# Optimization experiments

Hardware: AMD Instinct MI355X
Metric: run time of the kernel (lower is better)

The kernel has to match this reference:

```python
import jax, jax.numpy as jnp
import numpy as np

NVOC, NIN, NHID = 10000, 1024, 256
T, B = 128, 64


def setup_inputs() -> dict:
    key = jax.random.key(0)
    ks = jax.random.split(key, 12)

    def nrm(k, shape, s=0.05):
        return (jax.random.normal(k, shape) * s).astype(jnp.float32)

    z = lambda *s: jnp.zeros(s, jnp.float32)
    att_scale = 2.0 / np.sqrt(NHID)
    return {
        "tokens": jax.random.randint(ks[0], (T, B), 0, NVOC),
        "E": nrm(ks[1], (NVOC, NIN), 0.1),            # embedding table
        "Wih1": nrm(ks[2], (3 * NHID, NIN)),          # GRU1 input weights (r,z,n)
        "Whh1": nrm(ks[3], (3 * NHID, NHID)),
        "bih1": z(3 * NHID), "bhh1": z(3 * NHID),
        "Wih2": nrm(ks[4], (3 * NHID, NHID + NIN)),   # GRU2 input weights
        "Whh2": nrm(ks[5], (3 * NHID, NHID)),
        "bih2": z(3 * NHID), "bhh2": z(3 * NHID),
        "Wh": nrm(ks[6], (NHID, NHID)), "bh": z(NHID),   # attention linear_hid
        "Wi": nrm(ks[7], (NHID, NHID)), "bi": z(NHID),   # attention linear_input
        "w_att": nrm(ks[8], (NHID,), att_scale),          # attention score vector
        "Wd": nrm(ks[9], (NVOC, NHID), 0.1), "bd": z(NVOC),  # decoder
    }


def _gru_cell(h, xg, Whh, bhh):
    # xg: [B, 3H] precomputed input gates; PyTorch gate order (r, z, n)
    H = h.shape[-1]
    hg = h @ Whh.T + bhh
    r = jax.nn.sigmoid(xg[:, :H] + hg[:, :H])
    zt = jax.nn.sigmoid(xg[:, H:2 * H] + hg[:, H:2 * H])
    n = jnp.tanh(xg[:, 2 * H:] + r * hg[:, 2 * H:])
    return (1.0 - zt) * n + zt * h


def reference(tokens, E, Wih1, Whh1, bih1, bhh1, Wih2, Whh2, bih2, bhh2,
              Wh, bh, Wi, bi, w_att, Wd, bd):
    Tn, Bn = tokens.shape
    H = Whh1.shape[-1]
    emb = E[tokens]                                  # [T,B,NIN] (dropout = eval identity)

    # ---- rnn_1 over full sequence ----
    xg1 = emb @ Wih1.T + bih1                        # [T,B,3H]
    def step1(h, xg_t):
        h_new = _gru_cell(h, xg_t, Whh1, bhh1)
        return h_new, h_new
    h1, out1 = jax.lax.scan(step1, jnp.zeros((Bn, H), emb.dtype), xg1)
    # h1: final hidden [B,H]; out1: [T,B,H]

    # linear_hid on rnn_1 outputs (prefix slices of this equal per-step recompute)
    proj = out1 @ Wh.T + bh                          # [T,B,H]
    tidx = jnp.arange(Tn)
    neg_inf = jnp.asarray(-jnp.inf, proj.dtype)

    # ---- decode loop with growing-window additive attention ----
    def step2(h2, inputs):
        t, emb_t = inputs
        q = h2 @ Wi.T + bi                           # [B,H]
        scores = jnp.sum(jnp.tanh(proj + q[None]) * w_att, axis=2)   # [T,B]
        scores = jnp.where(tidx[:, None] <= t, scores, neg_inf)
        energy = jax.nn.softmax(scores, axis=0)      # [T,B], prefix softmax
        # hidden[:i+1] with nlayers=1 is always the [1,B,H] final rnn_1 hidden
        state = jnp.sum(energy[:, :, None] * h1[None], axis=0)       # [B,H]
        x = jnp.concatenate([state, emb_t], axis=1)  # [B, H+NIN]
        xg = x @ Wih2.T + bih2
        h2_new = _gru_cell(h2, xg, Whh2, bhh2)
        return h2_new, h2_new                        # pred == new hidden (1-layer GRU)

    _, preds = jax.lax.scan(step2, jnp.zeros((Bn, H), emb.dtype), (tidx, emb))
    # decoder (dropout = identity in eval)
    logits = preds @ Wd.T + bd                       # [T,B,NVOC]
    return logits, h1[None]                          # hidden returned as [1,B,H]
```

## Files before the change

### kernel.cpp

```cpp
#include <hip/hip_runtime.h>
#include <cstdint>
#include <cstddef>

#define DI __device__ __forceinline__

typedef short bf16x8 __attribute__((ext_vector_type(8)));
typedef float f32x4  __attribute__((ext_vector_type(4)));
typedef _Float16 half2v __attribute__((ext_vector_type(2)));

typedef const uint32_t __attribute__((address_space(1)))* gptr_t;
typedef uint32_t       __attribute__((address_space(3)))* lptr_t;

DI void load_lds16(const void* g, void* l_wave_uniform) {
#if __has_builtin(__builtin_amdgcn_global_load_lds)
  __builtin_amdgcn_global_load_lds((gptr_t)g, (lptr_t)l_wave_uniform, 16, 0, 0);
#else
  int lane = threadIdx.x & 63;
  *(uint4*)((char*)l_wave_uniform + lane * 16) = *(const uint4*)g;
#endif
}

DI ushort f2bf(float f) {
  uint32_t u = __builtin_bit_cast(uint32_t, f);
  u += 0x7fffu + ((u >> 16) & 1u);
  return (ushort)(u >> 16);
}

DI half2v h2cast(uint32_t u) { return __builtin_bit_cast(half2v, u); }

#if __has_builtin(__builtin_amdgcn_fdot2)
#define FDOT2(a, b, c) __builtin_amdgcn_fdot2((a), (b), (c), false)
#else
DI float fdot2_fb(half2v a, half2v b, float c) {
  return c + (float)a.x * (float)b.x + (float)a.y * (float)b.y;
}
#define FDOT2(a, b, c) fdot2_fb((a), (b), (c))
#endif


__global__ void cvt_w1cat(const float* __restrict__ W1, const float* __restrict__ W2,
                          ushort* __restrict__ dst) {
  int idx = blockIdx.x * 256 + threadIdx.x;
  int e = idx * 4;
  int row = e >> 10;
  int col = e & 1023;
  const float* src = (row < 768) ? (W1 + (size_t)row * 1024 + col)
                                 : (W2 + (size_t)(row - 768) * 1280 + 256 + col);
  float4 f = *(const float4*)src;
  ushort4 o; o.x = f2bf(f.x); o.y = f2bf(f.y); o.z = f2bf(f.z); o.w = f2bf(f.w);
  *(ushort4*)(dst + e) = o;
}

__global__ void cvt_wd(const float* __restrict__ Wd, ushort* __restrict__ dst) {
  int idx = blockIdx.x * 256 + threadIdx.x;
  int e = idx * 4;
  int row = e >> 8;
  int col = e & 255;
  ushort4 o;
  if (row < 10000) {
    float4 f = *(const float4*)(Wd + (size_t)row * 256 + col);
    o.x = f2bf(f.x); o.y = f2bf(f.y); o.z = f2bf(f.z); o.w = f2bf(f.w);
  } else {
    o.x = 0; o.y = 0; o.z = 0; o.w = 0;
  }
  *(ushort4*)(dst + e) = o;
}

__global__ void cvt_whh(const float* __restrict__ W, uint32_t* __restrict__ dst) {
  int idx = blockIdx.x * 256 + threadIdx.x;
  int row = idx >> 7;
  int p = idx & 127;
  float2 f = *(const float2*)(W + (size_t)row * 256 + p * 2);
  half2v h; h.x = (_Float16)f.x; h.y = (_Float16)f.y;
  dst[idx] = __builtin_bit_cast(uint32_t, h);
}

__global__ void gather_emb(const int* __restrict__ tok, const float* __restrict__ E,
                           ushort* __restrict__ emb) {
  int row = blockIdx.x;
  int t = threadIdx.x;
  int v = tok[row];
  float4 f = *((const float4*)(E + (size_t)v * 1024) + t);
  ushort4 o; o.x = f2bf(f.x); o.y = f2bf(f.y); o.z = f2bf(f.z); o.w = f2bf(f.w);
  *((ushort4*)(emb + (size_t)row * 1024) + t) = o;
}

template <bool BIAS, bool GUARD>
__global__ __launch_bounds__(256) void gemm_bt(
    const ushort* __restrict__ A, const ushort* __restrict__ B,
    float* __restrict__ C, const float* __restrict__ bias, int M, int K, int Nout) {
  __shared__ __align__(16) ushort As[128 * 64];
  __shared__ __align__(16) ushort Bs[128 * 64];
  const int t = threadIdx.x;
  const int wave = t >> 6, lane = t & 63;
  const int m0 = blockIdx.x * 128, n0 = blockIdx.y * 128;
  const int RM = (wave >> 1) * 64, RN = (wave & 1) * 64;
  const int lm = lane & 15, kg = lane >> 4;

  f32x4 acc[4][4] = {};

  for (int k0 = 0; k0 < K; k0 += 64) {
#pragma unroll
    for (int i = 0; i < 4; ++i) {
      int off = i * 4096 + t * 16;
      int row = off >> 7;
      int colb = off & 127;
      int ub = i * 4096 + wave * 1024;
      const ushort* ga = A + (size_t)(m0 + row) * K + k0 + (colb >> 1);
      load_lds16(ga, (char*)As + ub);
      const ushort* gb = B + (size_t)(n0 + row) * K + k0 + (colb >> 1);
      load_lds16(gb, (char*)Bs + ub);
    }
    __syncthreads();
#pragma unroll
    for (int kk = 0; kk < 64; kk += 32) {
      bf16x8 af[4], bfr[4];
#pragma unroll
      for (int i = 0; i < 4; ++i) {
        af[i]  = *(const bf16x8*)(As + (RM + i * 16 + lm) * 64 + kk + kg * 8);
        bfr[i] = *(const bf16x8*)(Bs + (RN + i * 16 + lm) * 64 + kk + kg * 8);
      }
#pragma unroll
      for (int i = 0; i < 4; ++i)
#pragma unroll
        for (int j = 0; j < 4; ++j)
          acc[i][j] = __builtin_amdgcn_mfma_f32_16x16x32_bf16(af[i], bfr[j], acc[i][j], 0, 0, 0);
    }
    __syncthreads();
  }

  const int rg = lane >> 4;
#pragma unroll
  for (int i = 0; i < 4; ++i) {
    int grow = m0 + RM + i * 16 + rg * 4;
#pragma unroll
    for (int j = 0; j < 4; ++j) {
      int gcol = n0 + RN + j * 16 + lm;
      if (GUARD && gcol >= Nout) continue;
      float bv = BIAS ? bias[gcol] : 0.f;
#pragma unroll
      for (int r = 0; r < 4; ++r)
        C[(size_t)(grow + r) * Nout + gcol] = acc[i][j][r] + bv;
    }
  }
}

__global__ __launch_bounds__(768, 3) void gru_scan(
    const uint32_t* __restrict__ Wpk,
    const float* __restrict__ xg_all,
    int xg_off,
    const float* __restrict__ bih, const float* __restrict__ bhh,
    const float* __restrict__ Wih2,
    const float* __restrict__ h1in,
    float* __restrict__ hfin_ws,
    float* __restrict__ hfin_out,
    ushort* __restrict__ preds)
{
  const int b = blockIdx.x;
  const int j = threadIdx.x;
  __shared__ __align__(16) uint32_t hpk[128];
  __shared__ float hf[256];
  __shared__ float rz[512];

  uint4 w[32];
  {
    const uint4* wp = (const uint4*)(Wpk + (size_t)j * 128);
#pragma unroll
    for (int i = 0; i < 32; ++i) w[i] = wp[i];
  }
  float xbase = bih[j];
  const float bhhj = bhh[j];
  if (Wih2) {
    const float4* wr = (const float4*)(Wih2 + (size_t)j * 1280);
    const float4* hb = (const float4*)(h1in + b * 256);
    float s = 0.f;
#pragma unroll 4
    for (int k = 0; k < 64; ++k) {
      float4 a = wr[k], c = hb[k];
      s += a.x * c.x + a.y * c.y + a.z * c.z + a.w * c.w;
    }
    xbase += s;
  }
  if (j < 128) hpk[j] = 0u;
  if (j < 256) hf[j] = 0.f;
  __syncthreads();

  for (int t = 0; t < 128; ++t) {
    float a0 = 0.f, a1 = 0.f, a2 = 0.f, a3 = 0.f;
#pragma unroll
    for (int i = 0; i < 32; ++i) {
      uint4 hv = ((const uint4*)hpk)[i];
      a0 = FDOT2(h2cast(w[i].x), h2cast(hv.x), a0);
      a1 = FDOT2(h2cast(w[i].y), h2cast(hv.y), a1);
      a2 = FDOT2(h2cast(w[i].z), h2cast(hv.z), a2);
      a3 = FDOT2(h2cast(w[i].w), h2cast(hv.w), a3);
    }
    float hg = (a0 + a1) + (a2 + a3) + bhhj;
    float xgv = xg_all[(size_t)(t * 64 + b) * 1536 + xg_off + j] + xbase;

    if (j < 512) rz[j] = 1.f / (1.f + __expf(-(xgv + hg)));
    __syncthreads();
    if (j >= 512) {
      int j2 = j - 512;
      float r = rz[j2], z = rz[256 + j2];
      float x2 = xgv + r * hg;
      x2 = fminf(fmaxf(x2, -15.f), 15.f);
      float e = __expf(-2.f * x2);
      float n = (1.f - e) / (1.f + e);
      float hnew = (1.f - z) * n + z * hf[j2];
      hf[j2] = hnew;
      if (preds) preds[(size_t)(t * 64 + b) * 256 + j2] = f2bf(hnew);
    }
    __syncthreads();
    if (j < 128) {
      half2v hh; hh.x = (_Float16)hf[2 * j]; hh.y = (_Float16)hf[2 * j + 1];
      hpk[j] = __builtin_bit_cast(uint32_t, hh);
    }
    __syncthreads();
  }

  if (j < 256) {
    if (hfin_ws)  hfin_ws[b * 256 + j] = hf[j];
    if (hfin_out) hfin_out[b * 256 + j] = hf[j];
  }
}

extern "C" void kernel_launch(void* const* d_in, const int* in_sizes, int n_in,
                              void* d_out, int out_size, void* d_ws, size_t ws_size,
                              hipStream_t stream) {
  const int*   tokens = (const int*)d_in[0];
  const float* E      = (const float*)d_in[1];
  const float* Wih1   = (const float*)d_in[2];
  const float* Whh1   = (const float*)d_in[3];
  const float* bih1   = (const float*)d_in[4];
  const float* bhh1   = (const float*)d_in[5];
  const float* Wih2   = (const float*)d_in[6];
  const float* Whh2   = (const float*)d_in[7];
  const float* bih2   = (const float*)d_in[8];
  const float* bhh2   = (const float*)d_in[9];
  const float* Wd     = (const float*)d_in[15];
  const float* bd     = (const float*)d_in[16];
  float* out = (float*)d_out;

  char* ws = (char*)d_ws;
  ushort*   emb   = (ushort*)  (ws + 0);
  ushort*   w1cat = (ushort*)  (ws + 16777216);
  float*    xg    = (float*)   (ws + 19922944);
  ushort*   wdb   = (ushort*)  (ws + 70254592);
  uint32_t* whh1p = (uint32_t*)(ws + 75431936);
  uint32_t* whh2p = (uint32_t*)(ws + 75825152);
  float*    h1    = (float*)   (ws + 76218368);
  ushort*   preds = (ushort*)  (ws + 76283904);

  cvt_w1cat<<<1536, 256, 0, stream>>>(Wih1, Wih2, w1cat);
  cvt_wd<<<2528, 256, 0, stream>>>(Wd, wdb);
  cvt_whh<<<384, 256, 0, stream>>>(Whh1, whh1p);
  cvt_whh<<<384, 256, 0, stream>>>(Whh2, whh2p);
  gather_emb<<<8192, 256, 0, stream>>>(tokens, E, emb);

  dim3 g1(64, 12);
  gemm_bt<false, false><<<g1, 256, 0, stream>>>(emb, w1cat, xg, nullptr, 8192, 1024, 1536);

  gru_scan<<<64, 768, 0, stream>>>(whh1p, xg, 0, bih1, bhh1,
                                   nullptr, nullptr, h1, out + 81920000, nullptr);
  gru_scan<<<64, 768, 0, stream>>>(whh2p, xg, 768, bih2, bhh2,
                                   Wih2, h1, nullptr, nullptr, preds);

  dim3 g2(64, 79);
  gemm_bt<true, true><<<g2, 256, 0, stream>>>(preds, wdb, out, bd, 8192, 256, 10000);
}
```

Before: 916.3 us.

## Swizzle GEMM LDS layout and cut GRU scan barriers with register state

The GEMM now stores LDS tiles with an XOR swizzle on 16-byte column groups, so MFMA fragment reads avoid bank conflicts. The GRU scan keeps the hidden state in registers instead of shared memory and packs the fp16 pairs with a wave shuffle. This removes one of the three barriers per timestep. It also prefetches the next timestep's input gate value so the global load latency overlaps the recurrent dot products. Register pressure rises slightly in a kernel already holding 128 weight registers per thread.

New measurement: 887.4 us. 3.2% less time.

```diff
diff --git a/kernel.cpp b/kernel.cpp
--- a/kernel.cpp
+++ b/kernel.cpp
@@ -104,21 +104,25 @@
     for (int i = 0; i < 4; ++i) {
       int off = i * 4096 + t * 16;
       int row = off >> 7;
-      int colb = off & 127;
+      int physc = (off >> 4) & 7;
+      int gc = physc ^ (row & 7);
       int ub = i * 4096 + wave * 1024;
-      const ushort* ga = A + (size_t)(m0 + row) * K + k0 + (colb >> 1);
+      const ushort* ga = A + (size_t)(m0 + row) * K + k0 + gc * 8;
       load_lds16(ga, (char*)As + ub);
-      const ushort* gb = B + (size_t)(n0 + row) * K + k0 + (colb >> 1);
+      const ushort* gb = B + (size_t)(n0 + row) * K + k0 + gc * 8;
       load_lds16(gb, (char*)Bs + ub);
     }
     __syncthreads();
 #pragma unroll
     for (int kk = 0; kk < 64; kk += 32) {
+      const int lc = (kk >> 3) + kg;
       bf16x8 af[4], bfr[4];
 #pragma unroll
       for (int i = 0; i < 4; ++i) {
-        af[i]  = *(const bf16x8*)(As + (RM + i * 16 + lm) * 64 + kk + kg * 8);
-        bfr[i] = *(const bf16x8*)(Bs + (RN + i * 16 + lm) * 64 + kk + kg * 8);
+        int ra = RM + i * 16 + lm;
+        int rb = RN + i * 16 + lm;
+        af[i]  = *(const bf16x8*)(As + ra * 64 + ((lc ^ (ra & 7)) << 3));
+        bfr[i] = *(const bf16x8*)(Bs + rb * 64 + ((lc ^ (rb & 7)) << 3));
       }
 #pragma unroll
       for (int i = 0; i < 4; ++i)
@@ -159,33 +163,40 @@
   const int b = blockIdx.x;
   const int j = threadIdx.x;
   __shared__ __align__(16) uint32_t hpk[128];
-  __shared__ float hf[256];
   __shared__ float rz[512];
 
-  uint4 w[32];
-  {
-    const uint4* wp = (const uint4*)(Wpk + (size_t)j * 128);
-#pragma unroll
-    for (int i = 0; i < 32; ++i) w[i] = wp[i];
-  }
   float xbase = bih[j];
   const float bhhj = bhh[j];
   if (Wih2) {
     const float4* wr = (const float4*)(Wih2 + (size_t)j * 1280);
     const float4* hb = (const float4*)(h1in + b * 256);
     float s = 0.f;
-#pragma unroll 4
+#pragma unroll 2
     for (int k = 0; k < 64; ++k) {
       float4 a = wr[k], c = hb[k];
       s += a.x * c.x + a.y * c.y + a.z * c.z + a.w * c.w;
     }
     xbase += s;
   }
+
+  uint4 w[32];
+  {
+    const uint4* wp = (const uint4*)(Wpk + (size_t)j * 128);
+#pragma unroll
+    for (int i = 0; i < 32; ++i) w[i] = wp[i];
+  }
+
   if (j < 128) hpk[j] = 0u;
-  if (j < 256) hf[j] = 0.f;
+  float hprev = 0.f;
   __syncthreads();
 
+  const float* xgp = xg_all + (size_t)b * 1536 + xg_off + j;
+  float xcur = xgp[0];
+
   for (int t = 0; t < 128; ++t) {
+    int tn = (t + 1 < 128) ? t + 1 : 127;
+    float xnext = xgp[(size_t)tn * 98304];
+
     float a0 = 0.f, a1 = 0.f, a2 = 0.f, a3 = 0.f;
 #pragma unroll
     for (int i = 0; i < 32; ++i) {
@@ -196,7 +207,7 @@
       a3 = FDOT2(h2cast(w[i].w), h2cast(hv.w), a3);
     }
     float hg = (a0 + a1) + (a2 + a3) + bhhj;
-    float xgv = xg_all[(size_t)(t * 64 + b) * 1536 + xg_off + j] + xbase;
+    float xgv = xcur + xbase;
 
     if (j < 512) rz[j] = 1.f / (1.f + __expf(-(xgv + hg)));
     __syncthreads();
@@ -207,21 +218,23 @@
       x2 = fminf(fmaxf(x2, -15.f), 15.f);
       float e = __expf(-2.f * x2);
       float n = (1.f - e) / (1.f + e);
-      float hnew = (1.f - z) * n + z * hf[j2];
-      hf[j2] = hnew;
+      float hnew = (1.f - z) * n + z * hprev;
+      hprev = hnew;
       if (preds) preds[(size_t)(t * 64 + b) * 256 + j2] = f2bf(hnew);
-    }
-    __syncthreads();
-    if (j < 128) {
-      half2v hh; hh.x = (_Float16)hf[2 * j]; hh.y = (_Float16)hf[2 * j + 1];
-      hpk[j] = __builtin_bit_cast(uint32_t, hh);
-    }
-    __syncthreads();
-  }
-
-  if (j < 256) {
-    if (hfin_ws)  hfin_ws[b * 256 + j] = hf[j];
-    if (hfin_out) hfin_out[b * 256 + j] = hf[j];
+      float hup = __shfl_down(hnew, 1);
+      if (!(j2 & 1)) {
+        half2v hh; hh.x = (_Float16)hnew; hh.y = (_Float16)hup;
+        hpk[j2 >> 1] = __builtin_bit_cast(uint32_t, hh);
+      }
+    }
+    xcur = xnext;
+    __syncthreads();
+  }
+
+  if (j >= 512) {
+    int j2 = j - 512;
+    if (hfin_ws)  hfin_ws[b * 256 + j2] = hprev;
+    if (hfin_out) hfin_out[b * 256 + j2] = hprev;
   }
 }
 
```
